# Kernel optimization log

Measured on AMD Instinct MI355X. Metric: run time of the kernel, lower is better.

## Reference

```python
import jax, jax.numpy as jnp
import numpy as np

EPS = 1e-6
KH, KW = 3, 3  # (freq, time) depthwise kernel


def setup_inputs() -> dict:
    key = jax.random.key(0)
    ks = jax.random.split(key, 5)
    B, C, F, T = 4, 128, 128, 512
    H = 2 * C  # hidden = channels * expansion
    x = jax.random.normal(ks[0], (B, C, F, T), dtype=jnp.float32)
    g_norm = jnp.ones((C,), dtype=jnp.float32)
    w_in = jax.random.normal(ks[1], (2 * H, C), dtype=jnp.float32) * 0.05
    b_in = jnp.zeros((2 * H,), dtype=jnp.float32)
    w_dw = jax.random.normal(ks[2], (H, 1, KH, KW), dtype=jnp.float32) * 0.1
    b_dw = jnp.zeros((H,), dtype=jnp.float32)
    w_out = jax.random.normal(ks[3], (C, H), dtype=jnp.float32) * 0.05
    b_out = jnp.zeros((C,), dtype=jnp.float32)
    return {"x": x, "g_norm": g_norm, "w_in": w_in, "b_in": b_in,
            "w_dw": w_dw, "b_dw": b_dw, "w_out": w_out, "b_out": b_out}


def _rmsnorm2d(x, g):
    # normalize over channel dim (dim=1), learned per-channel scale
    ms = jnp.mean(jnp.square(x), axis=1, keepdims=True)
    return x * jax.lax.rsqrt(ms + EPS) * g[None, :, None, None]


def reference(x, g_norm, w_in, b_in, w_dw, b_dw, w_out, b_out):
    B, C, F, T = x.shape
    H = w_dw.shape[0]
    y = _rmsnorm2d(x, g_norm)
    # in_proj: 1x1 conv == channel GEMM; output 2H channels, chunk into a, b
    ab = jnp.einsum('oc,bcft->boft', w_in, y) + b_in[None, :, None, None]
    a, b = ab[:, :H], ab[:, H:]
    y = a * jax.nn.sigmoid(b)  # GLU gate
    # causal depthwise conv: 'same' pad on freq, left-pad (KW-1) on time
    y = jax.lax.conv_general_dilated(
        y, w_dw, window_strides=(1, 1),
        padding=[((KH - 1) // 2, KH // 2), (KW - 1, 0)],
        dimension_numbers=('NCHW', 'OIHW', 'NCHW'),
        feature_group_count=H) + b_dw[None, :, None, None]
    y = jax.nn.silu(y)
    # out_proj: 1x1 conv + residual
    out = jnp.einsum('co,boft->bcft', w_out, y) + b_out[None, :, None, None]
    return x + out
```

## Files before the change

kernel.cpp:

```cpp
#include <hip/hip_runtime.h>
#include <hip/hip_bf16.h>

using bf16x8 = __attribute__((ext_vector_type(8))) __bf16;
using f32x4  = __attribute__((ext_vector_type(4))) float;
typedef unsigned short ushort8v __attribute__((ext_vector_type(8)));
typedef unsigned short ushort4v __attribute__((ext_vector_type(4)));

#define B_ 4
#define C_ 128
#define F_ 128
#define T_ 512
#define H_ 256
#define FT_ 65536
#define M_ 262144

static __device__ __forceinline__ unsigned short bf16bits(float f) {
    __hip_bfloat16 h = __float2bfloat16(f);
    return *(unsigned short*)&h;
}

static __device__ __forceinline__ f32x4 ld4(const __hip_bfloat16* p) {
    ushort4v u = *(const ushort4v*)p;
    f32x4 r;
#pragma unroll
    for (int i = 0; i < 4; ++i) {
        union { unsigned int ui; float f; } cv;
        cv.ui = ((unsigned int)u[i]) << 16;
        r[i] = cv.f;
    }
    return r;
}

static __device__ __forceinline__ f32x4 zero4() {
    f32x4 r = {0.f, 0.f, 0.f, 0.f};
    return r;
}

__global__ __launch_bounds__(256) void k_cast(const float* __restrict__ w_in,
                                              const float* __restrict__ w_out,
                                              __hip_bfloat16* __restrict__ wib,
                                              __hip_bfloat16* __restrict__ wob) {
    int i = blockIdx.x * 256 + threadIdx.x;
    if (i < 512 * 128) wib[i] = __float2bfloat16(w_in[i]);
    if (i < 128 * 256) wob[i] = __float2bfloat16(w_out[i]);
}

__global__ __launch_bounds__(256) void k_rms(const float* __restrict__ x,
                                             const float* __restrict__ gn,
                                             __hip_bfloat16* __restrict__ yt) {
    __shared__ float xs[128][129];
    __shared__ float ssqs[2][128];
    __shared__ float scl[128];
    const int bid = blockIdx.x;
    const int tc = bid & 3;
    const int bf = bid >> 2;
    const int b = bf >> 7, f = bf & 127;
    const int t0 = tc * 128;
    const int th = threadIdx.x;
    const int tl = th & 127, ch = th >> 7;
    const size_t base = (size_t)b * (C_ * FT_) + (size_t)f * T_ + t0;
    float ssq = 0.f;
    for (int c = ch; c < 128; c += 2) {
        float v = x[base + (size_t)c * FT_ + tl];
        xs[c][tl] = v;
        ssq += v * v;
    }
    ssqs[ch][tl] = ssq;
    __syncthreads();
    if (th < 128) {
        float ms = (ssqs[0][th] + ssqs[1][th]) * (1.f / 128.f);
        scl[th] = rsqrtf(ms + 1e-6f);
    }
    __syncthreads();
    const int c = th & 127, tp = th >> 7;
    const float gc = gn[c];
    const size_t m0 = (size_t)bf * T_ + t0;
    for (int tt = 0; tt < 128; tt += 2) {
        const int t = tt + tp;
        float v = xs[c][t] * scl[t] * gc;
        yt[(m0 + t) * 128 + c] = __float2bfloat16(v);
    }
}

__global__ __launch_bounds__(256) void k_gemm1(const __hip_bfloat16* __restrict__ yt,
                                               const __hip_bfloat16* __restrict__ wib,
                                               const float* __restrict__ b_in,
                                               __hip_bfloat16* __restrict__ gbuf) {
    __shared__ __hip_bfloat16 Al[128][136];
    __shared__ __hip_bfloat16 Bl[128][136];
    const int m0 = blockIdx.x * 128;
    const int hb = blockIdx.y * 64;
    const int th = threadIdx.x;
    {
        const int row = th >> 1, half = th & 1;
        const ushort8v* srcA = (const ushort8v*)(yt + (size_t)(m0 + row) * 128 + half * 64);
        ushort8v* dstA = (ushort8v*)(&Al[row][half * 64]);
#pragma unroll
        for (int i = 0; i < 8; ++i) dstA[i] = srcA[i];
        const int q = row >> 5, r = row & 31;
        const int o = (r < 16) ? (hb + q * 16 + r) : (256 + hb + q * 16 + (r - 16));
        const ushort8v* srcB = (const ushort8v*)(wib + (size_t)o * 128 + half * 64);
        ushort8v* dstB = (ushort8v*)(&Bl[row][half * 64]);
#pragma unroll
        for (int i = 0; i < 8; ++i) dstB[i] = srcB[i];
    }
    __syncthreads();
    const int lane = th & 63, wave = th >> 6;
    const int wm = wave >> 1, wn = wave & 1;
    const int lr = lane & 15, lg = lane >> 4;
    f32x4 acc[4][4] = {};
#pragma unroll
    for (int kk = 0; kk < 4; ++kk) {
        bf16x8 af[4], bq[4];
#pragma unroll
        for (int ma = 0; ma < 4; ++ma)
            af[ma] = *(const bf16x8*)(&Al[wm * 64 + ma * 16 + lr][kk * 32 + lg * 8]);
#pragma unroll
        for (int na = 0; na < 4; ++na)
            bq[na] = *(const bf16x8*)(&Bl[wn * 64 + na * 16 + lr][kk * 32 + lg * 8]);
#pragma unroll
        for (int ma = 0; ma < 4; ++ma)
#pragma unroll
            for (int na = 0; na < 4; ++na)
                acc[ma][na] = __builtin_amdgcn_mfma_f32_16x16x32_bf16(af[ma], bq[na], acc[ma][na], 0, 0, 0);
    }
    __syncthreads();
    __hip_bfloat16 (*gl)[68] = (__hip_bfloat16(*)[68])(&Bl[0][0]);
#pragma unroll
    for (int p = 0; p < 2; ++p) {
        const int q = wn * 2 + p;
        const int oa = hb + q * 16 + lr;
        const float ba = b_in[oa];
        const float bb = b_in[256 + oa];
#pragma unroll
        for (int ma = 0; ma < 4; ++ma) {
            f32x4 va = acc[ma][2 * p];
            f32x4 vb = acc[ma][2 * p + 1];
#pragma unroll
            for (int j = 0; j < 4; ++j) {
                float aa = va[j] + ba;
                float bv = vb[j] + bb;
                float gv = aa / (1.f + __expf(-bv));
                gl[wm * 64 + ma * 16 + lg * 4 + j][wn * 32 + p * 16 + lr] = __float2bfloat16(gv);
            }
        }
    }
    __syncthreads();
#pragma unroll
    for (int pass = 0; pass < 8; ++pass) {
        const int ml = pass * 16 + (th >> 4);
        const int h4 = (th & 15) * 4;
        ushort4v v = *(const ushort4v*)(&gl[ml][h4]);
        *(ushort4v*)((unsigned short*)gbuf + (size_t)(m0 + ml) * 256 + hb + h4) = v;
    }
}

__global__ __launch_bounds__(256) void k_gemm2(const __hip_bfloat16* __restrict__ gbuf,
                                               const __hip_bfloat16* __restrict__ wob,
                                               const float* __restrict__ w_dw,
                                               const float* __restrict__ b_dw,
                                               const float* __restrict__ b_out,
                                               const float* __restrict__ x,
                                               float* __restrict__ out) {
    __shared__ __hip_bfloat16 Wl[128][136];
    __shared__ __hip_bfloat16 Sl[128][136];
    const int m0 = blockIdx.x * 128;
    const int th = threadIdx.x;
    const int bfrow = m0 >> 9;
    const int f = bfrow & 127;
    const int t0 = m0 & 511;
    const int lane = th & 63, wave = th >> 6;
    const int wc = wave >> 1, wn = wave & 1;
    const int lr = lane & 15, lg = lane >> 4;
    const bool hm = (f > 0), hp = (f < 127);
    const __hip_bfloat16* gc_ = gbuf + ((size_t)bfrow * 512) * 256;
    const __hip_bfloat16* gm_ = gc_ - (size_t)512 * 256;
    const __hip_bfloat16* gp_ = gc_ + (size_t)512 * 256;
    f32x4 acc[4][4] = {};
    for (int ks = 0; ks < 2; ++ks) {
        const int o0 = ks * 128;
        {
            const int row = th >> 1, half = th & 1;
            const ushort8v* srcW = (const ushort8v*)(wob + (size_t)row * 256 + o0 + half * 64);
            ushort8v* dstW = (ushort8v*)(&Wl[row][half * 64]);
#pragma unroll
            for (int i = 0; i < 8; ++i) dstW[i] = srcW[i];
        }
        {
            const int o4 = o0 + ((th & 31) << 2);
            const int mh8 = th >> 5;
            const int tb = t0 + mh8 * 16;
            f32x4 wv[9], a0[3], a1[3], a2[3], bias;
#pragma unroll
            for (int i = 0; i < 9; ++i)
#pragma unroll
                for (int c = 0; c < 4; ++c) wv[i][c] = w_dw[(o4 + c) * 9 + i];
#pragma unroll
            for (int c = 0; c < 4; ++c) bias[c] = b_dw[o4 + c];
#pragma unroll
            for (int kI = 0; kI < 2; ++kI) {
                const int t = tb - 2 + kI;
                const bool tv = (t >= 0);
                const size_t off = (size_t)t * 256 + o4;
                a0[kI] = (tv && hm) ? ld4(gm_ + off) : zero4();
                a1[kI] = tv        ? ld4(gc_ + off) : zero4();
                a2[kI] = (tv && hp) ? ld4(gp_ + off) : zero4();
            }
#pragma unroll 4
            for (int k = 0; k < 16; ++k) {
                const int t = tb + k;
                const size_t off = (size_t)t * 256 + o4;
                a0[2] = hm ? ld4(gm_ + off) : zero4();
                a1[2] = ld4(gc_ + off);
                a2[2] = hp ? ld4(gp_ + off) : zero4();
                f32x4 av = bias;
#pragma unroll
                for (int j = 0; j < 3; ++j) {
                    av += wv[j] * a0[j];
                    av += wv[3 + j] * a1[j];
                    av += wv[6 + j] * a2[j];
                }
                ushort4v uo;
#pragma unroll
                for (int c = 0; c < 4; ++c) {
                    float sv = av[c] / (1.f + __expf(-av[c]));
                    uo[c] = bf16bits(sv);
                }
                *(ushort4v*)(&Sl[mh8 * 16 + k][(th & 31) << 2]) = uo;
                a0[0] = a0[1]; a0[1] = a0[2];
                a1[0] = a1[1]; a1[1] = a1[2];
                a2[0] = a2[1]; a2[1] = a2[2];
            }
        }
        __syncthreads();
#pragma unroll
        for (int kk = 0; kk < 4; ++kk) {
            bf16x8 af[4], bq[4];
#pragma unroll
            for (int ca = 0; ca < 4; ++ca)
                af[ca] = *(const bf16x8*)(&Wl[wc * 64 + ca * 16 + lr][kk * 32 + lg * 8]);
#pragma unroll
            for (int na = 0; na < 4; ++na)
                bq[na] = *(const bf16x8*)(&Sl[wn * 64 + na * 16 + lr][kk * 32 + lg * 8]);
#pragma unroll
            for (int ca = 0; ca < 4; ++ca)
#pragma unroll
                for (int na = 0; na < 4; ++na)
                    acc[ca][na] = __builtin_amdgcn_mfma_f32_16x16x32_bf16(af[ca], bq[na], acc[ca][na], 0, 0, 0);
        }
        __syncthreads();
    }
    const size_t sbase = (size_t)(m0 >> 16) * (C_ * FT_);
#pragma unroll
    for (int ca = 0; ca < 4; ++ca) {
        const int cbase = wc * 64 + ca * 16 + lg * 4;
#pragma unroll
        for (int na = 0; na < 4; ++na) {
            const int m = m0 + wn * 64 + na * 16 + lr;
            const size_t sp = sbase + (size_t)(m & 65535);
#pragma unroll
            for (int j = 0; j < 4; ++j) {
                const int cc = cbase + j;
                const size_t idx = sp + (size_t)cc * FT_;
                out[idx] = acc[ca][na][j] + b_out[cc] + x[idx];
            }
        }
    }
}

extern "C" void kernel_launch(void* const* d_in, const int* in_sizes, int n_in,
                              void* d_out, int out_size, void* d_ws, size_t ws_size,
                              hipStream_t stream) {
    const float* x      = (const float*)d_in[0];
    const float* g_norm = (const float*)d_in[1];
    const float* w_in   = (const float*)d_in[2];
    const float* b_in   = (const float*)d_in[3];
    const float* w_dw   = (const float*)d_in[4];
    const float* b_dw   = (const float*)d_in[5];
    const float* w_out  = (const float*)d_in[6];
    const float* b_out  = (const float*)d_in[7];
    float* out = (float*)d_out;

    char* ws = (char*)d_ws;
    __hip_bfloat16* gbuf = (__hip_bfloat16*)ws;
    __hip_bfloat16* ybuf = (__hip_bfloat16*)(ws + (size_t)134217728);
    __hip_bfloat16* wib  = (__hip_bfloat16*)(ws + (size_t)134217728 + 67108864);
    __hip_bfloat16* wob  = wib + 512 * 128;

    k_cast<<<dim3(256), dim3(256), 0, stream>>>(w_in, w_out, wib, wob);
    k_rms<<<dim3(2048), dim3(256), 0, stream>>>(x, g_norm, ybuf);
    k_gemm1<<<dim3(2048, 4), dim3(256), 0, stream>>>(ybuf, wib, b_in, gbuf);
    k_gemm2<<<dim3(2048), dim3(256), 0, stream>>>(gbuf, wob, w_dw, b_dw, b_out, x, out);
}
```

Baseline: 634.4 us.

## Split depthwise conv into own kernel and load GEMM operands directly from global

Splits the depthwise conv + SiLU out of the second GEMM into a separate k_dw kernel that writes an intermediate bf16 buffer. Both GEMMs drop LDS staging and read MFMA fragments straight from global memory. gemm1's grid is reordered so consecutive blocks share the same activation rows, and k_dw uses a swizzled block order. This removes the in-GEMM conv recomputation and the LDS sync overhead, but adds an extra 128MB write and read round trip and depends on uncoalesced fragment loads being served from cache.

```diff
diff --git a/kernel.cpp b/kernel.cpp
--- a/kernel.cpp
+++ b/kernel.cpp
@@ -86,46 +86,36 @@
                                                const __hip_bfloat16* __restrict__ wib,
                                                const float* __restrict__ b_in,
                                                __hip_bfloat16* __restrict__ gbuf) {
-    __shared__ __hip_bfloat16 Al[128][136];
-    __shared__ __hip_bfloat16 Bl[128][136];
-    const int m0 = blockIdx.x * 128;
-    const int hb = blockIdx.y * 64;
-    const int th = threadIdx.x;
-    {
-        const int row = th >> 1, half = th & 1;
-        const ushort8v* srcA = (const ushort8v*)(yt + (size_t)(m0 + row) * 128 + half * 64);
-        ushort8v* dstA = (ushort8v*)(&Al[row][half * 64]);
-#pragma unroll
-        for (int i = 0; i < 8; ++i) dstA[i] = srcA[i];
-        const int q = row >> 5, r = row & 31;
-        const int o = (r < 16) ? (hb + q * 16 + r) : (256 + hb + q * 16 + (r - 16));
-        const ushort8v* srcB = (const ushort8v*)(wib + (size_t)o * 128 + half * 64);
-        ushort8v* dstB = (ushort8v*)(&Bl[row][half * 64]);
-#pragma unroll
-        for (int i = 0; i < 8; ++i) dstB[i] = srcB[i];
-    }
-    __syncthreads();
+    __shared__ __hip_bfloat16 gl[128][68];
+    const int hb = blockIdx.x * 64;
+    const int m0 = blockIdx.y * 128;
+    const int th = threadIdx.x;
     const int lane = th & 63, wave = th >> 6;
     const int wm = wave >> 1, wn = wave & 1;
     const int lr = lane & 15, lg = lane >> 4;
+    const unsigned short* ytu = (const unsigned short*)yt;
+    const unsigned short* wibu = (const unsigned short*)wib;
     f32x4 acc[4][4] = {};
 #pragma unroll
     for (int kk = 0; kk < 4; ++kk) {
         bf16x8 af[4], bq[4];
 #pragma unroll
-        for (int ma = 0; ma < 4; ++ma)
-            af[ma] = *(const bf16x8*)(&Al[wm * 64 + ma * 16 + lr][kk * 32 + lg * 8]);
-#pragma unroll
-        for (int na = 0; na < 4; ++na)
-            bq[na] = *(const bf16x8*)(&Bl[wn * 64 + na * 16 + lr][kk * 32 + lg * 8]);
+        for (int ma = 0; ma < 4; ++ma) {
+            const int row = m0 + wm * 64 + ma * 16 + lr;
+            af[ma] = *(const bf16x8*)(ytu + (size_t)row * 128 + kk * 32 + lg * 8);
+        }
+#pragma unroll
+        for (int na = 0; na < 4; ++na) {
+            const int q = wn * 2 + (na >> 1);
+            const int o = ((na & 1) ? 256 : 0) + hb + q * 16 + lr;
+            bq[na] = *(const bf16x8*)(wibu + (size_t)o * 128 + kk * 32 + lg * 8);
+        }
 #pragma unroll
         for (int ma = 0; ma < 4; ++ma)
 #pragma unroll
             for (int na = 0; na < 4; ++na)
                 acc[ma][na] = __builtin_amdgcn_mfma_f32_16x16x32_bf16(af[ma], bq[na], acc[ma][na], 0, 0, 0);
     }
-    __syncthreads();
-    __hip_bfloat16 (*gl)[68] = (__hip_bfloat16(*)[68])(&Bl[0][0]);
 #pragma unroll
     for (int p = 0; p < 2; ++p) {
         const int q = wn * 2 + p;
@@ -155,100 +145,96 @@
     }
 }
 
-__global__ __launch_bounds__(256) void k_gemm2(const __hip_bfloat16* __restrict__ gbuf,
+__global__ __launch_bounds__(256) void k_dw(const __hip_bfloat16* __restrict__ g,
+                                            const float* __restrict__ w_dw,
+                                            const float* __restrict__ b_dw,
+                                            __hip_bfloat16* __restrict__ s) {
+    const int orig = ((blockIdx.x & 7) << 8) + (blockIdx.x >> 3);
+    const int bf = orig >> 2, tc = orig & 3;
+    const int f = bf & 127;
+    const int th = threadIdx.x;
+    const int o4 = (th & 63) << 2;
+    const int tb = tc * 128 + (th >> 6) * 32;
+    const bool hm = (f > 0), hp = (f < 127);
+    const __hip_bfloat16* gc_ = g + (size_t)bf * 512 * 256;
+    const __hip_bfloat16* gm_ = gc_ - (size_t)512 * 256;
+    const __hip_bfloat16* gp_ = gc_ + (size_t)512 * 256;
+    f32x4 wv[9], bias;
+#pragma unroll
+    for (int i = 0; i < 9; ++i)
+#pragma unroll
+        for (int c = 0; c < 4; ++c) wv[i][c] = w_dw[(o4 + c) * 9 + i];
+#pragma unroll
+    for (int c = 0; c < 4; ++c) bias[c] = b_dw[o4 + c];
+    f32x4 a0[3], a1[3], a2[3];
+#pragma unroll
+    for (int kI = 0; kI < 2; ++kI) {
+        const int t = tb - 2 + kI;
+        const bool tv = (t >= 0);
+        const size_t off = (size_t)t * 256 + o4;
+        a0[kI] = (tv && hm) ? ld4(gm_ + off) : zero4();
+        a1[kI] = tv        ? ld4(gc_ + off) : zero4();
+        a2[kI] = (tv && hp) ? ld4(gp_ + off) : zero4();
+    }
+    unsigned short* su = (unsigned short*)s;
+#pragma unroll 4
+    for (int k = 0; k < 32; ++k) {
+        const int t = tb + k;
+        const size_t off = (size_t)t * 256 + o4;
+        a0[2] = hm ? ld4(gm_ + off) : zero4();
+        a1[2] = ld4(gc_ + off);
+        a2[2] = hp ? ld4(gp_ + off) : zero4();
+        f32x4 av = bias;
+#pragma unroll
+        for (int j = 0; j < 3; ++j) {
+            av += wv[j] * a0[j];
+            av += wv[3 + j] * a1[j];
+            av += wv[6 + j] * a2[j];
+        }
+        ushort4v uo;
+#pragma unroll
+        for (int c = 0; c < 4; ++c) {
+            float d = 1.f + __expf(-av[c]);
+            uo[c] = bf16bits(av[c] * __builtin_amdgcn_rcpf(d));
+        }
+        *(ushort4v*)(su + ((size_t)bf * 512 + t) * 256 + o4) = uo;
+        a0[0] = a0[1]; a0[1] = a0[2];
+        a1[0] = a1[1]; a1[1] = a1[2];
+        a2[0] = a2[1]; a2[1] = a2[2];
+    }
+}
+
+__global__ __launch_bounds__(256) void k_gemm2(const __hip_bfloat16* __restrict__ s,
                                                const __hip_bfloat16* __restrict__ wob,
-                                               const float* __restrict__ w_dw,
-                                               const float* __restrict__ b_dw,
                                                const float* __restrict__ b_out,
                                                const float* __restrict__ x,
                                                float* __restrict__ out) {
-    __shared__ __hip_bfloat16 Wl[128][136];
-    __shared__ __hip_bfloat16 Sl[128][136];
     const int m0 = blockIdx.x * 128;
     const int th = threadIdx.x;
-    const int bfrow = m0 >> 9;
-    const int f = bfrow & 127;
-    const int t0 = m0 & 511;
     const int lane = th & 63, wave = th >> 6;
     const int wc = wave >> 1, wn = wave & 1;
     const int lr = lane & 15, lg = lane >> 4;
-    const bool hm = (f > 0), hp = (f < 127);
-    const __hip_bfloat16* gc_ = gbuf + ((size_t)bfrow * 512) * 256;
-    const __hip_bfloat16* gm_ = gc_ - (size_t)512 * 256;
-    const __hip_bfloat16* gp_ = gc_ + (size_t)512 * 256;
+    const unsigned short* su = (const unsigned short*)s;
+    const unsigned short* wu = (const unsigned short*)wob;
     f32x4 acc[4][4] = {};
-    for (int ks = 0; ks < 2; ++ks) {
-        const int o0 = ks * 128;
-        {
-            const int row = th >> 1, half = th & 1;
-            const ushort8v* srcW = (const ushort8v*)(wob + (size_t)row * 256 + o0 + half * 64);
-            ushort8v* dstW = (ushort8v*)(&Wl[row][half * 64]);
-#pragma unroll
-            for (int i = 0; i < 8; ++i) dstW[i] = srcW[i];
-        }
-        {
-            const int o4 = o0 + ((th & 31) << 2);
-            const int mh8 = th >> 5;
-            const int tb = t0 + mh8 * 16;
-            f32x4 wv[9], a0[3], a1[3], a2[3], bias;
-#pragma unroll
-            for (int i = 0; i < 9; ++i)
-#pragma unroll
-                for (int c = 0; c < 4; ++c) wv[i][c] = w_dw[(o4 + c) * 9 + i];
-#pragma unroll
-            for (int c = 0; c < 4; ++c) bias[c] = b_dw[o4 + c];
-#pragma unroll
-            for (int kI = 0; kI < 2; ++kI) {
-                const int t = tb - 2 + kI;
-                const bool tv = (t >= 0);
-                const size_t off = (size_t)t * 256 + o4;
-                a0[kI] = (tv && hm) ? ld4(gm_ + off) : zero4();
-                a1[kI] = tv        ? ld4(gc_ + off) : zero4();
-                a2[kI] = (tv && hp) ? ld4(gp_ + off) : zero4();
-            }
-#pragma unroll 4
-            for (int k = 0; k < 16; ++k) {
-                const int t = tb + k;
-                const size_t off = (size_t)t * 256 + o4;
-                a0[2] = hm ? ld4(gm_ + off) : zero4();
-                a1[2] = ld4(gc_ + off);
-                a2[2] = hp ? ld4(gp_ + off) : zero4();
-                f32x4 av = bias;
-#pragma unroll
-                for (int j = 0; j < 3; ++j) {
-                    av += wv[j] * a0[j];
-                    av += wv[3 + j] * a1[j];
-                    av += wv[6 + j] * a2[j];
-                }
-                ushort4v uo;
-#pragma unroll
-                for (int c = 0; c < 4; ++c) {
-                    float sv = av[c] / (1.f + __expf(-av[c]));
-                    uo[c] = bf16bits(sv);
-                }
-                *(ushort4v*)(&Sl[mh8 * 16 + k][(th & 31) << 2]) = uo;
-                a0[0] = a0[1]; a0[1] = a0[2];
-                a1[0] = a1[1]; a1[1] = a1[2];
-                a2[0] = a2[1]; a2[1] = a2[2];
-            }
-        }
-        __syncthreads();
-#pragma unroll
-        for (int kk = 0; kk < 4; ++kk) {
-            bf16x8 af[4], bq[4];
-#pragma unroll
-            for (int ca = 0; ca < 4; ++ca)
-                af[ca] = *(const bf16x8*)(&Wl[wc * 64 + ca * 16 + lr][kk * 32 + lg * 8]);
+#pragma unroll
+    for (int kk = 0; kk < 8; ++kk) {
+        bf16x8 af[4], bq[4];
+#pragma unroll
+        for (int ca = 0; ca < 4; ++ca) {
+            const int row = wc * 64 + ca * 16 + lr;
+            af[ca] = *(const bf16x8*)(wu + (size_t)row * 256 + kk * 32 + lg * 8);
+        }
+#pragma unroll
+        for (int na = 0; na < 4; ++na) {
+            const int m = m0 + wn * 64 + na * 16 + lr;
+            bq[na] = *(const bf16x8*)(su + (size_t)m * 256 + kk * 32 + lg * 8);
+        }
+#pragma unroll
+        for (int ca = 0; ca < 4; ++ca)
 #pragma unroll
             for (int na = 0; na < 4; ++na)
-                bq[na] = *(const bf16x8*)(&Sl[wn * 64 + na * 16 + lr][kk * 32 + lg * 8]);
-#pragma unroll
-            for (int ca = 0; ca < 4; ++ca)
-#pragma unroll
-                for (int na = 0; na < 4; ++na)
-                    acc[ca][na] = __builtin_amdgcn_mfma_f32_16x16x32_bf16(af[ca], bq[na], acc[ca][na], 0, 0, 0);
-        }
-        __syncthreads();
+                acc[ca][na] = __builtin_amdgcn_mfma_f32_16x16x32_bf16(af[ca], bq[na], acc[ca][na], 0, 0, 0);
     }
     const size_t sbase = (size_t)(m0 >> 16) * (C_ * FT_);
 #pragma unroll
@@ -283,12 +269,14 @@
 
     char* ws = (char*)d_ws;
     __hip_bfloat16* gbuf = (__hip_bfloat16*)ws;
-    __hip_bfloat16* ybuf = (__hip_bfloat16*)(ws + (size_t)134217728);
-    __hip_bfloat16* wib  = (__hip_bfloat16*)(ws + (size_t)134217728 + 67108864);
+    __hip_bfloat16* sbuf = (__hip_bfloat16*)(ws + (size_t)134217728);
+    __hip_bfloat16* ybuf = (__hip_bfloat16*)(ws + (size_t)134217728 + 67108864);
+    __hip_bfloat16* wib  = (__hip_bfloat16*)(ws + (size_t)268435456);
     __hip_bfloat16* wob  = wib + 512 * 128;
 
     k_cast<<<dim3(256), dim3(256), 0, stream>>>(w_in, w_out, wib, wob);
     k_rms<<<dim3(2048), dim3(256), 0, stream>>>(x, g_norm, ybuf);
-    k_gemm1<<<dim3(2048, 4), dim3(256), 0, stream>>>(ybuf, wib, b_in, gbuf);
-    k_gemm2<<<dim3(2048), dim3(256), 0, stream>>>(gbuf, wob, w_dw, b_dw, b_out, x, out);
-}
+    k_gemm1<<<dim3(4, 2048), dim3(256), 0, stream>>>(ybuf, wib, b_in, gbuf);
+    k_dw<<<dim3(2048), dim3(256), 0, stream>>>(gbuf, w_dw, b_dw, sbuf);
+    k_gemm2<<<dim3(2048), dim3(256), 0, stream>>>(sbuf, wob, b_out, x, out);
+}
```

New measurement: 702.9 us. +10.8%, slower.
